# Performance work log

Hardware: AMD Instinct MI355X
Metric: run time of the kernel (lower is better)

The kernel has to match this reference:

```python
import jax, jax.numpy as jnp
import numpy as np

K = 32
BN_EPS = 1e-5


def _edgeconv(x, W, b):
    # x: [N, f] one point cloud; dynamic kNN in feature space (self included,
    # matching torch_geometric knn), edge feature [x_i, x_j - x_i], linear MLP,
    # max aggregation over the k neighbors.
    sq = jnp.sum(x * x, axis=1)                      # [N]
    dist = sq[:, None] + sq[None, :] - 2.0 * (x @ x.T)  # [N, N] squared dists
    _, idx = jax.lax.top_k(-dist, K)                 # [N, K] nearest (incl. self)
    xj = x[idx]                                      # [N, K, f]
    xi = jnp.broadcast_to(x[:, None, :], xj.shape)   # [N, K, f]
    e = jnp.concatenate([xi, xj - xi], axis=-1)      # [N, K, 2f]
    m = jnp.einsum('nkf,fo->nko', e, W) + b          # [N, K, o]
    return jnp.max(m, axis=1)                        # [N, o]


def _relu_bn(y, gamma, beta):
    # Sequential(ReLU(), BatchNorm1d(o)) in training mode over flattened nodes.
    a = jax.nn.relu(y)                               # [B, N, o]
    B, N, o = a.shape
    flat = a.reshape(B * N, o)
    mean = jnp.mean(flat, axis=0)
    var = jnp.var(flat, axis=0)
    norm = (flat - mean) * jax.lax.rsqrt(var + BN_EPS)
    return (norm * gamma + beta).reshape(B, N, o)


def setup_inputs() -> dict:
    key = jax.random.key(0)
    ks = jax.random.split(key, 4)
    B, N, fin = 8, 4096, 3
    x = jax.random.normal(ks[0], (B, N, fin), dtype=jnp.float32)
    target = jax.random.normal(ks[1], (B, N, fin), dtype=jnp.float32)
    # MLP(2*i, o) weights for layer dims (3->64), (64->64), (64->3)
    W1 = jax.random.normal(ks[2], (6, 64), dtype=jnp.float32) * (1.0 / np.sqrt(6))
    b1 = jnp.zeros((64,), jnp.float32)
    g1 = jnp.ones((64,), jnp.float32)
    be1 = jnp.zeros((64,), jnp.float32)
    W2 = jax.random.normal(ks[3], (128, 64), dtype=jnp.float32) * (1.0 / np.sqrt(128))
    b2 = jnp.zeros((64,), jnp.float32)
    g2 = jnp.ones((64,), jnp.float32)
    be2 = jnp.zeros((64,), jnp.float32)
    W3 = jax.random.normal(jax.random.fold_in(key, 7), (128, 3), dtype=jnp.float32) * (1.0 / np.sqrt(128))
    b3 = jnp.zeros((3,), jnp.float32)
    return {"x": x, "target": target, "W1": W1, "b1": b1, "g1": g1, "be1": be1,
            "W2": W2, "b2": b2, "g2": g2, "be2": be2, "W3": W3, "b3": b3}


def reference(x, target, W1, b1, g1, be1, W2, b2, g2, be2, W3, b3):
    ec = jax.vmap(_edgeconv, in_axes=(0, None, None))
    h = ec(x, W1, b1)                 # [B, N, 64]
    h = _relu_bn(h, g1, be1)
    h = ec(h, W2, b2)                 # [B, N, 64]
    h = _relu_bn(h, g2, be2)
    h = ec(h, W3, b3)                 # [B, N, 3], last activation = Identity
    loss = jnp.mean((h - target) ** 2)
    return (h, loss)
```

## Files before the change

kernel.cpp:

```cpp
#include <hip/hip_runtime.h>
#include <cstdint>
#include <cstddef>

static constexpr int NPTS  = 4096;
static constexpr int NB    = 8;
static constexpr int NROWS = NB * NPTS;
static constexpr int KNN   = 32;
static constexpr int CAP   = 256;
static constexpr int HCAP  = 128;

typedef __attribute__((ext_vector_type(8))) short  bf16x8;
typedef __attribute__((ext_vector_type(4))) float  f32x4;

__device__ __forceinline__ unsigned long long shfl_xor_u64(unsigned long long v, int m) {
  int lo = __shfl_xor((int)(unsigned)(v & 0xFFFFFFFFULL), m, 64);
  int hi = __shfl_xor((int)(unsigned)(v >> 32), m, 64);
  return ((unsigned long long)(unsigned)hi << 32) | (unsigned)lo;
}
__device__ __forceinline__ unsigned long long shfl_u64(unsigned long long v, int src) {
  int lo = __shfl((int)(unsigned)(v & 0xFFFFFFFFULL), src, 64);
  int hi = __shfl((int)(unsigned)(v >> 32), src, 64);
  return ((unsigned long long)(unsigned)hi << 32) | (unsigned)lo;
}

__device__ __forceinline__ unsigned f2o(float f) {
  unsigned u = __float_as_uint(f);
  return (u & 0x80000000u) ? ~u : (u | 0x80000000u);
}
__device__ __forceinline__ float o2f(unsigned o) {
  unsigned u = (o & 0x80000000u) ? (o ^ 0x80000000u) : ~o;
  return __uint_as_float(u);
}

__global__ __launch_bounds__(256) void sqnorm_kernel(const float* __restrict__ x,
                                                     float* __restrict__ sq, int F) {
  int t = blockIdx.x * 256 + threadIdx.x;
  if (t >= NROWS) return;
  const float* p = x + (size_t)t * F;
  float s = 0.f;
  for (int f = 0; f < F; ++f) s = fmaf(p[f], p[f], s);
  sq[t] = s;
}

__global__ __launch_bounds__(256) void split_kernel(const float* __restrict__ x,
                                                    unsigned short* __restrict__ hi,
                                                    unsigned short* __restrict__ lo,
                                                    int total) {
  int t = blockIdx.x * 256 + threadIdx.x;
  if (t >= total) return;
  float v = x[t];
  unsigned u = __float_as_uint(v);
  unsigned h = (u + 0x7FFFu + ((u >> 16) & 1u)) >> 16;
  float hf = __uint_as_float(h << 16);
  float r = v - hf;
  unsigned ur = __float_as_uint(r);
  unsigned l = (ur + 0x7FFFu + ((ur >> 16) & 1u)) >> 16;
  hi[t] = (unsigned short)h;
  lo[t] = (unsigned short)l;
}

__global__ __launch_bounds__(256) void batchmax_kernel(const float* __restrict__ sq,
                                                       float* __restrict__ sqmax) {
  int b = blockIdx.x, t = threadIdx.x;
  float m = 0.f;
  for (int i = t; i < NPTS; i += 256) m = fmaxf(m, sq[b * NPTS + i]);
  for (int off = 32; off >= 1; off >>= 1) m = fmaxf(m, __shfl_xor(m, off, 64));
  __shared__ float ls[4];
  if ((t & 63) == 0) ls[t >> 6] = m;
  __syncthreads();
  if (t == 0) sqmax[b] = fmaxf(fmaxf(ls[0], ls[1]), fmaxf(ls[2], ls[3]));
}

__global__ __launch_bounds__(256, 4)
void knn_screen(const unsigned short* __restrict__ hi,
                const unsigned short* __restrict__ lo,
                const float* __restrict__ sq,
                const float* __restrict__ sqmax,
                int* __restrict__ gcnt,
                unsigned short* __restrict__ glist) {
  constexpr int FPS = 72;
  __shared__ __attribute__((aligned(16))) unsigned short chi[128 * FPS];
  __shared__ __attribute__((aligned(16))) unsigned short clo[128 * FPS];
  __shared__ float csq[128];

  const int t = threadIdx.x, wave = t >> 6, lane = t & 63;
  const int l16 = lane & 15, quad = lane >> 4;
  const int bid = blockIdx.x;
  const int b    = bid & 7;
  const int half = (bid >> 3) & 1;
  const int i0w  = ((bid >> 4) << 6) + (wave << 4);
  const int cb   = half << 11;
  const size_t base = (size_t)b * NPTS;
  const unsigned short* hib = hi + base * 64;
  const unsigned short* lob = lo + base * 64;
  const float* sqb = sq + base;
  const float sqm = sqmax[b];

  bf16x8 ahi[2], alo[2];
#pragma unroll
  for (int kb = 0; kb < 2; ++kb) {
    ahi[kb] = *(const bf16x8*)(hib + (size_t)(i0w + l16) * 64 + kb * 32 + quad * 8);
    alo[kb] = *(const bf16x8*)(lob + (size_t)(i0w + l16) * 64 + kb * 32 + quad * 8);
  }
  float sqi4[4];
#pragma unroll
  for (int reg = 0; reg < 4; ++reg) sqi4[reg] = sqb[i0w + quad * 4 + reg];

  float t1[4], t2[4], t3[4], t4[4], tinf4[4];
  int cnt4[4] = {0, 0, 0, 0};
#pragma unroll
  for (int reg = 0; reg < 4; ++reg) {
    t1[reg] = 3.4e38f; t2[reg] = 3.4e38f; t3[reg] = 3.4e38f; t4[reg] = 3.4e38f;
    tinf4[reg] = 0.f;
  }

  for (int pass = 0; pass < 2; ++pass) {
    for (int tile = 0; tile < 16; ++tile) {
      __syncthreads();
#pragma unroll
      for (int p = 0; p < 4; ++p) {
        int id = t + p * 256;
        int r = id >> 3, c = id & 7;
        *(bf16x8*)&chi[r * FPS + c * 8] =
            *(const bf16x8*)(hib + (size_t)(cb + tile * 128 + r) * 64 + c * 8);
        *(bf16x8*)&clo[r * FPS + c * 8] =
            *(const bf16x8*)(lob + (size_t)(cb + tile * 128 + r) * 64 + c * 8);
      }
      if (t < 128) csq[t] = sqb[cb + tile * 128 + t];
      __syncthreads();

#pragma unroll 2
      for (int sub = 0; sub < 8; ++sub) {
        const int jl = sub * 16 + l16;
        bf16x8 bh0 = *(const bf16x8*)&chi[jl * FPS + quad * 8];
        bf16x8 bh1 = *(const bf16x8*)&chi[jl * FPS + 32 + quad * 8];
        bf16x8 bl0 = *(const bf16x8*)&clo[jl * FPS + quad * 8];
        bf16x8 bl1 = *(const bf16x8*)&clo[jl * FPS + 32 + quad * 8];
        f32x4 acc = {0.f, 0.f, 0.f, 0.f};
        acc = __builtin_amdgcn_mfma_f32_16x16x32_bf16(ahi[0], bh0, acc, 0, 0, 0);
        acc = __builtin_amdgcn_mfma_f32_16x16x32_bf16(ahi[1], bh1, acc, 0, 0, 0);
        acc = __builtin_amdgcn_mfma_f32_16x16x32_bf16(ahi[0], bl0, acc, 0, 0, 0);
        acc = __builtin_amdgcn_mfma_f32_16x16x32_bf16(ahi[1], bl1, acc, 0, 0, 0);
        acc = __builtin_amdgcn_mfma_f32_16x16x32_bf16(alo[0], bh0, acc, 0, 0, 0);
        acc = __builtin_amdgcn_mfma_f32_16x16x32_bf16(alo[1], bh1, acc, 0, 0, 0);
        const float cs = csq[jl];
        const int jg = cb + tile * 128 + jl;
#pragma unroll
        for (int reg = 0; reg < 4; ++reg) {
          float d = fmaf(-2.f, acc[reg], sqi4[reg] + cs);
          if (pass == 0) {
            float m1 = fminf(d,  t1[reg]); float M1 = fmaxf(d,  t1[reg]);
            float m2 = fminf(M1, t2[reg]); float M2 = fmaxf(M1, t2[reg]);
            float m3 = fminf(M2, t3[reg]); float M3 = fmaxf(M2, t3[reg]);
            t1[reg] = m1; t2[reg] = m2; t3[reg] = m3;
            t4[reg] = fminf(M3, t4[reg]);
          } else {
            bool keep = d <= tinf4[reg];
            unsigned long long mask = __ballot(keep);
            unsigned qm = (unsigned)((mask >> (quad * 16)) & 0xFFFFULL);
            int rank = __popc(qm & ((1u << l16) - 1u));
            if (keep) {
              int pos = cnt4[reg] + rank;
              if (pos < HCAP)
                glist[(size_t)(base + i0w + quad * 4 + reg) * CAP + half * HCAP + pos] =
                    (unsigned short)jg;
            }
            cnt4[reg] += __popc(qm);
          }
        }
      }
    }
    if (pass == 0) {
#pragma unroll
      for (int reg = 0; reg < 4; ++reg) {
        unsigned c0s = f2o(t1[reg]);
        unsigned c1s = f2o(t2[reg]);
        unsigned c2s = f2o(t3[reg]);
        unsigned c3s = f2o(t4[reg]);
        unsigned prefix = 0;
        int need = 32;
        for (int bit = 31; bit >= 0; --bit) {
          unsigned hm = (bit == 31) ? 0u : ~((1u << (bit + 1)) - 1u);
          bool a0 = (((c0s ^ prefix) & hm) == 0u) && (((c0s >> bit) & 1u) == 0u);
          bool a1 = (((c1s ^ prefix) & hm) == 0u) && (((c1s >> bit) & 1u) == 0u);
          bool a2 = (((c2s ^ prefix) & hm) == 0u) && (((c2s >> bit) & 1u) == 0u);
          bool a3 = (((c3s ^ prefix) & hm) == 0u) && (((c3s >> bit) & 1u) == 0u);
          unsigned long long b0 = __ballot(a0);
          unsigned long long b1 = __ballot(a1);
          unsigned long long b2 = __ballot(a2);
          unsigned long long b3 = __ballot(a3);
          int cnt0 = __popc((unsigned)((b0 >> (quad * 16)) & 0xFFFFULL))
                   + __popc((unsigned)((b1 >> (quad * 16)) & 0xFFFFULL))
                   + __popc((unsigned)((b2 >> (quad * 16)) & 0xFFFFULL))
                   + __popc((unsigned)((b3 >> (quad * 16)) & 0xFFFFULL));
          if (cnt0 < need) { need -= cnt0; prefix |= 1u << bit; }
        }
        float T = o2f(prefix);
        float eps = 6e-5f * (sqi4[reg] + sqm) + 1e-5f;
        tinf4[reg] = T + 2.f * eps;
      }
    }
  }

  if (l16 == 0) {
#pragma unroll
    for (int reg = 0; reg < 4; ++reg)
      gcnt[(base + i0w + quad * 4 + reg) * 2 + half] = cnt4[reg];
  }
}

__global__ __launch_bounds__(256, 2)
void knn_rerank(const float* __restrict__ x, const float* __restrict__ sq,
                const int* __restrict__ gcnt,
                const unsigned short* __restrict__ glist,
                unsigned short* __restrict__ idx_out) {
  const int t = threadIdx.x, wave = t >> 6, lane = t & 63;
  const int row = blockIdx.x * 4 + wave;
  const int b = row >> 12;
  const int i = row & (NPTS - 1);
  const float* xb  = x + (size_t)b * NPTS * 64;
  const float* sqb = sq + ((size_t)b << 12);

  const int n0 = gcnt[row * 2];
  const int n1 = gcnt[row * 2 + 1];
  if (n0 > HCAP || n1 > HCAP) return;

  const float sqi = sqb[i];
  float4 q[16];
#pragma unroll
  for (int c4 = 0; c4 < 16; ++c4)
    q[c4] = *(const float4*)(xb + (size_t)i * 64 + c4 * 4);

  const int n = n0 + n1;
  unsigned long long vk[4];
#pragma unroll
  for (int s = 0; s < 4; ++s) {
    int li = s * 64 + lane;
    unsigned long long v = 0xFFFFFFFFFFFULL;
    if (li < n) {
      int sl = (li < n0) ? li : (HCAP + (li - n0));
      int j = glist[(size_t)row * CAP + sl];
      const float4* xj = (const float4*)(xb + (size_t)j * 64);
      float dot = 0.f;
#pragma unroll
      for (int c4 = 0; c4 < 16; ++c4) {
        float4 c = xj[c4];
        dot = fmaf(q[c4].x, c.x, dot);
        dot = fmaf(q[c4].y, c.y, dot);
        dot = fmaf(q[c4].z, c.z, dot);
        dot = fmaf(q[c4].w, c.w, dot);
      }
      float d = fmaf(-2.f, dot, sqi + sqb[j]);
      unsigned u  = __float_as_uint(d);
      unsigned ck = (u & 0x80000000u) ? ~u : (u | 0x80000000u);
      v = ((unsigned long long)ck << 12) | (unsigned)j;
    }
    vk[s] = v;
  }
  unsigned long long prefix = 0;
  int need = 32;
  for (int bit = 43; bit >= 0; --bit) {
    unsigned long long hm = (bit == 43) ? 0ULL
        : (~((1ULL << (bit + 1)) - 1ULL) & 0xFFFFFFFFFFFULL);
    int cnt0 = 0;
#pragma unroll
    for (int s = 0; s < 4; ++s) {
      bool a = ((vk[s] ^ prefix) & hm) == 0ULL;
      bool z = ((vk[s] >> bit) & 1ULL) == 0ULL;
      cnt0 += (int)__popcll(__ballot(a && z));
    }
    if (cnt0 < need) { need -= cnt0; prefix |= 1ULL << bit; }
  }
  int prev = 0;
#pragma unroll
  for (int s = 0; s < 4; ++s) {
    bool sel = vk[s] <= prefix;
    unsigned long long m = __ballot(sel);
    int rank = (int)__popcll(m & ((1ULL << lane) - 1ULL));
    if (sel)
      idx_out[(size_t)row * KNN + prev + rank] =
          (unsigned short)(vk[s] & 0xFFFULL);
    prev += (int)__popcll(m);
  }
}

__global__ __launch_bounds__(256)
void knn_rerank_fb(const float* __restrict__ x, const float* __restrict__ sq,
                   const int* __restrict__ gcnt,
                   unsigned short* __restrict__ idx_out) {
  __shared__ unsigned long long fsurv[4][128];
  const int t = threadIdx.x, wave = t >> 6, lane = t & 63;
  const int row = blockIdx.x * 4 + wave;
  const int b = row >> 12;
  const int i = row & (NPTS - 1);

  const int n0 = gcnt[row * 2];
  const int n1 = gcnt[row * 2 + 1];
  if (n0 <= HCAP && n1 <= HCAP) return;

  const float* xb  = x + (size_t)b * NPTS * 64;
  const float* sqb = sq + ((size_t)b << 12);
  const float sqi = sqb[i];

  float4 q[16];
#pragma unroll
  for (int c4 = 0; c4 < 16; ++c4)
    q[c4] = *(const float4*)(xb + (size_t)i * 64 + c4 * 4);

  unsigned mnf = 0xFFFFFFFFu;
  for (int c0 = 0; c0 < NPTS; c0 += 64) {
    const int j = c0 + lane;
    const float4* xj = (const float4*)(xb + (size_t)j * 64);
    float dot = 0.f;
#pragma unroll
    for (int c4 = 0; c4 < 16; ++c4) {
      float4 c = xj[c4];
      dot = fmaf(q[c4].x, c.x, dot);
      dot = fmaf(q[c4].y, c.y, dot);
      dot = fmaf(q[c4].z, c.z, dot);
      dot = fmaf(q[c4].w, c.w, dot);
    }
    float d = fmaf(-2.f, dot, sqi + sqb[j]);
    unsigned u  = __float_as_uint(d);
    unsigned ck = (u & 0x80000000u) ? ~u : (u | 0x80000000u);
    mnf = ck < mnf ? ck : mnf;
  }
  unsigned tau32;
  {
    const unsigned v = mnf;
    unsigned prefix32 = 0;
    int need = 32;
    int act = 1;
    for (int bit = 31; bit >= 0; --bit) {
      const unsigned bv = (v >> bit) & 1u;
      unsigned long long m0 = __ballot(act && (bv == 0u));
      int c0n = (int)__popcll(m0);
      if (c0n >= need) {
        act = act && (bv == 0u);
      } else {
        need -= c0n;
        act = act && (bv == 1u);
        prefix32 |= (1u << bit);
      }
    }
    tau32 = prefix32;
  }
  int cnt = 0;
  for (int c0 = 0; c0 < NPTS; c0 += 64) {
    const int j = c0 + lane;
    const float4* xj = (const float4*)(xb + (size_t)j * 64);
    float dot = 0.f;
#pragma unroll
    for (int c4 = 0; c4 < 16; ++c4) {
      float4 c = xj[c4];
      dot = fmaf(q[c4].x, c.x, dot);
      dot = fmaf(q[c4].y, c.y, dot);
      dot = fmaf(q[c4].z, c.z, dot);
      dot = fmaf(q[c4].w, c.w, dot);
    }
    float d = fmaf(-2.f, dot, sqi + sqb[j]);
    unsigned u  = __float_as_uint(d);
    unsigned ck = (u & 0x80000000u) ? ~u : (u | 0x80000000u);
    bool keep = ck <= tau32;
    unsigned long long mask = __ballot(keep);
    if (mask != 0ULL) {
      int rank = (int)__popcll(mask & ((1ULL << lane) - 1ULL));
      if (keep) {
        int pos = cnt + rank;
        if (pos < 128)
          fsurv[wave][pos] = ((unsigned long long)ck << 12) | (unsigned)j;
      }
      cnt += (int)__popcll(mask);
    }
  }
  if (cnt <= 128) {
    unsigned long long vk0 = (lane      < cnt) ? fsurv[wave][lane]      : 0xFFFFFFFFFFFULL;
    unsigned long long vk1 = (lane + 64 < cnt) ? fsurv[wave][lane + 64] : 0xFFFFFFFFFFFULL;
    unsigned long long prefix = 0;
    int need = 32;
    for (int bit = 43; bit >= 0; --bit) {
      unsigned long long hm = (bit == 43) ? 0ULL
          : (~((1ULL << (bit + 1)) - 1ULL) & 0xFFFFFFFFFFFULL);
      bool a0 = (((vk0 ^ prefix) & hm) == 0ULL) && (((vk0 >> bit) & 1ULL) == 0ULL);
      bool a1 = (((vk1 ^ prefix) & hm) == 0ULL) && (((vk1 >> bit) & 1ULL) == 0ULL);
      int cnt0 = (int)__popcll(__ballot(a0)) + (int)__popcll(__ballot(a1));
      if (cnt0 < need) { need -= cnt0; prefix |= 1ULL << bit; }
    }
    bool sel0 = vk0 <= prefix;
    unsigned long long m0 = __ballot(sel0);
    int rank0 = (int)__popcll(m0 & ((1ULL << lane) - 1ULL));
    if (sel0)
      idx_out[(size_t)row * KNN + rank0] = (unsigned short)(vk0 & 0xFFFULL);
    int prev = (int)__popcll(m0);
    bool sel1 = vk1 <= prefix;
    unsigned long long m1 = __ballot(sel1);
    int rank1 = (int)__popcll(m1 & ((1ULL << lane) - 1ULL));
    if (sel1)
      idx_out[(size_t)row * KNN + prev + rank1] = (unsigned short)(vk1 & 0xFFFULL);
  } else {
    unsigned long long ent = (0xFFFFFFFFFFFULL << 5) | (unsigned long long)(lane & 31);
    unsigned long long M   = (0xFFFFFFFFFFFULL << 5) | 31ULL;
    for (int c0 = 0; c0 < NPTS; c0 += 64) {
      const int j = c0 + lane;
      const float4* xj = (const float4*)(xb + (size_t)j * 64);
      float dot = 0.f;
#pragma unroll
      for (int c4 = 0; c4 < 16; ++c4) {
        float4 c = xj[c4];
        dot = fmaf(q[c4].x, c.x, dot);
        dot = fmaf(q[c4].y, c.y, dot);
        dot = fmaf(q[c4].z, c.z, dot);
        dot = fmaf(q[c4].w, c.w, dot);
      }
      float d = fmaf(-2.f, dot, sqi + sqb[j]);
      unsigned u  = __float_as_uint(d);
      unsigned ck = (u & 0x80000000u) ? ~u : (u | 0x80000000u);
      unsigned long long cq = ((unsigned long long)ck << 12) | (unsigned)j;
      unsigned long long mask = __ballot(cq < (M >> 5));
      while (mask) {
        const int src = __builtin_ctzll(mask);
        mask &= mask - 1;
        const unsigned long long bq = shfl_u64(cq, src);
        if (bq < (M >> 5)) {
          const unsigned slot = (unsigned)(M & 31ULL);
          if ((unsigned)(lane & 31) == slot) ent = (bq << 5) | slot;
          unsigned long long v = ent;
#pragma unroll
          for (int off = 16; off >= 1; off >>= 1) {
            unsigned long long w2 = shfl_xor_u64(v, off);
            v = (v > w2) ? v : w2;
          }
          M = v;
        }
      }
    }
    if (lane < 32)
      idx_out[(size_t)row * KNN + lane] =
          (unsigned short)((ent >> 5) & 0xFFFULL);
  }
}

template <int F>
__global__ __launch_bounds__(256, 4) void knn_tiled(const float* __restrict__ x,
                                                    const float* __restrict__ sq,
                                                    unsigned short* __restrict__ idx_out) {
  constexpr int FP = 4;
  constexpr int TC = 256;
  constexpr int RPB = 32;
  constexpr int RPW = 8;
  constexpr int SCAP = 128;

  __shared__ __attribute__((aligned(16))) float qv[RPB][FP];
  __shared__ float qsq[RPB];
  __shared__ __attribute__((aligned(16))) float ct[TC][FP];
  __shared__ float csq[TC];
  __shared__ unsigned long long surv[RPB][SCAP];

  const int t    = threadIdx.x;
  const int wave = t >> 6;
  const int lane = t & 63;
  const int rowbase = blockIdx.x << 5;
  const int b     = rowbase >> 12;
  const int ibase = rowbase & (NPTS - 1);
  const float* xb  = x + (size_t)b * NPTS * F;
  const float* sqb = sq + (b << 12);

  if (t < RPB) {
    qv[t][0] = xb[(size_t)(ibase + t) * 3 + 0];
    qv[t][1] = xb[(size_t)(ibase + t) * 3 + 1];
    qv[t][2] = xb[(size_t)(ibase + t) * 3 + 2];
    qv[t][3] = 0.f;
    qsq[t] = sqb[ibase + t];
  }
  __syncthreads();

  const int r0 = wave << 3;
  float4 q[RPW];
  float sqi[RPW];
#pragma unroll
  for (int rr = 0; rr < RPW; ++rr) {
    q[rr] = *reinterpret_cast<const float4*>(&qv[r0 + rr][0]);
    sqi[rr] = qsq[r0 + rr];
  }

  unsigned mn[RPW];
#pragma unroll
  for (int rr = 0; rr < RPW; ++rr) mn[rr] = 0xFFFFFFFFu;

  for (int tile = 0; tile < NPTS / TC; ++tile) {
    __syncthreads();
    {
      int jg = tile * TC + t;
      ct[t][0] = xb[(size_t)jg * 3 + 0];
      ct[t][1] = xb[(size_t)jg * 3 + 1];
      ct[t][2] = xb[(size_t)jg * 3 + 2];
      ct[t][3] = 0.f;
      csq[t] = sqb[jg];
    }
    __syncthreads();

    float4 c0 = *reinterpret_cast<const float4*>(&ct[lane][0]);
    float4 c1 = *reinterpret_cast<const float4*>(&ct[lane + 64][0]);
    float4 c2 = *reinterpret_cast<const float4*>(&ct[lane + 128][0]);
    float4 c3 = *reinterpret_cast<const float4*>(&ct[lane + 192][0]);
    float cs[4];
#pragma unroll
    for (int s = 0; s < 4; ++s) cs[s] = csq[lane + 64 * s];

#pragma unroll
    for (int rr = 0; rr < RPW; ++rr) {
      float4 qq = q[rr];
      float dd[4];
      dd[0] = fmaf(qq.z, c0.z, fmaf(qq.y, c0.y, qq.x * c0.x));
      dd[1] = fmaf(qq.z, c1.z, fmaf(qq.y, c1.y, qq.x * c1.x));
      dd[2] = fmaf(qq.z, c2.z, fmaf(qq.y, c2.y, qq.x * c2.x));
      dd[3] = fmaf(qq.z, c3.z, fmaf(qq.y, c3.y, qq.x * c3.x));
#pragma unroll
      for (int s = 0; s < 4; ++s) {
        float d = fmaf(-2.f, dd[s], sqi[rr] + cs[s]);
        unsigned u  = __float_as_uint(d);
        unsigned ck = (u & 0x80000000u) ? ~u : (u | 0x80000000u);
        mn[rr] = ck < mn[rr] ? ck : mn[rr];
      }
    }
  }

  unsigned tau[RPW];
#pragma unroll
  for (int rr = 0; rr < RPW; ++rr) {
    const unsigned v = mn[rr];
    unsigned prefix = 0;
    int need = 32;
    int act = 1;
    for (int bit = 31; bit >= 0; --bit) {
      const unsigned bv = (v >> bit) & 1u;
      unsigned long long m0 = __ballot(act && (bv == 0u));
      int c0n = (int)__popcll(m0);
      if (c0n >= need) {
        act = act && (bv == 0u);
      } else {
        need -= c0n;
        act = act && (bv == 1u);
        prefix |= (1u << bit);
      }
    }
    tau[rr] = prefix;
  }

  int cnt[RPW];
#pragma unroll
  for (int rr = 0; rr < RPW; ++rr) cnt[rr] = 0;

  for (int tile = 0; tile < NPTS / TC; ++tile) {
    __syncthreads();
    {
      int jg = tile * TC + t;
      ct[t][0] = xb[(size_t)jg * 3 + 0];
      ct[t][1] = xb[(size_t)jg * 3 + 1];
      ct[t][2] = xb[(size_t)jg * 3 + 2];
      ct[t][3] = 0.f;
      csq[t] = sqb[jg];
    }
    __syncthreads();

    float4 c0 = *reinterpret_cast<const float4*>(&ct[lane][0]);
    float4 c1 = *reinterpret_cast<const float4*>(&ct[lane + 64][0]);
    float4 c2 = *reinterpret_cast<const float4*>(&ct[lane + 128][0]);
    float4 c3 = *reinterpret_cast<const float4*>(&ct[lane + 192][0]);
    float cs[4];
#pragma unroll
    for (int s = 0; s < 4; ++s) cs[s] = csq[lane + 64 * s];

#pragma unroll
    for (int rr = 0; rr < RPW; ++rr) {
      float4 qq = q[rr];
      float dd[4];
      dd[0] = fmaf(qq.z, c0.z, fmaf(qq.y, c0.y, qq.x * c0.x));
      dd[1] = fmaf(qq.z, c1.z, fmaf(qq.y, c1.y, qq.x * c1.x));
      dd[2] = fmaf(qq.z, c2.z, fmaf(qq.y, c2.y, qq.x * c2.x));
      dd[3] = fmaf(qq.z, c3.z, fmaf(qq.y, c3.y, qq.x * c3.x));
#pragma unroll
      for (int s = 0; s < 4; ++s) {
        float d = fmaf(-2.f, dd[s], sqi[rr] + cs[s]);
        unsigned u  = __float_as_uint(d);
        unsigned ck = (u & 0x80000000u) ? ~u : (u | 0x80000000u);
        bool keep = ck <= tau[rr];
        unsigned long long mask = __ballot(keep);
        if (mask != 0ULL) {
          int rank = (int)__popcll(mask & ((1ULL << lane) - 1ULL));
          if (keep) {
            int pos = cnt[rr] + rank;
            if (pos < SCAP)
              surv[r0 + rr][pos] =
                  ((unsigned long long)ck << 12) |
                  (unsigned)(tile * TC + s * 64 + lane);
          }
          cnt[rr] += (int)__popcll(mask);
        }
      }
    }
  }

#pragma unroll
  for (int rr = 0; rr < RPW; ++rr) {
    const int row = rowbase + r0 + rr;
    const int n = cnt[rr];
    if (n <= SCAP) {
      unsigned long long vk0 = (lane      < n) ? surv[r0 + rr][lane]      : 0xFFFFFFFFFFFULL;
      unsigned long long vk1 = (lane + 64 < n) ? surv[r0 + rr][lane + 64] : 0xFFFFFFFFFFFULL;
      unsigned long long prefix = 0;
      int need = 32;
      for (int bit = 43; bit >= 0; --bit) {
        unsigned long long hm = (bit == 43) ? 0ULL
            : (~((1ULL << (bit + 1)) - 1ULL) & 0xFFFFFFFFFFFULL);
        bool a0 = (((vk0 ^ prefix) & hm) == 0ULL) && (((vk0 >> bit) & 1ULL) == 0ULL);
        bool a1 = (((vk1 ^ prefix) & hm) == 0ULL) && (((vk1 >> bit) & 1ULL) == 0ULL);
        int cnt0 = (int)__popcll(__ballot(a0)) + (int)__popcll(__ballot(a1));
        if (cnt0 < need) { need -= cnt0; prefix |= 1ULL << bit; }
      }
      bool sel0 = vk0 <= prefix;
      unsigned long long m0 = __ballot(sel0);
      int rank0 = (int)__popcll(m0 & ((1ULL << lane) - 1ULL));
      if (sel0)
        idx_out[(row << 5) + rank0] = (unsigned short)(vk0 & 0xFFFULL);
      int prev = (int)__popcll(m0);
      bool sel1 = vk1 <= prefix;
      unsigned long long m1 = __ballot(sel1);
      int rank1 = (int)__popcll(m1 & ((1ULL << lane) - 1ULL));
      if (sel1)
        idx_out[(row << 5) + prev + rank1] = (unsigned short)(vk1 & 0xFFFULL);
    } else {
      unsigned long long ent = (0xFFFFFFFFFFFULL << 5) | (unsigned long long)(lane & 31);
      unsigned long long M   = (0xFFFFFFFFFFFULL << 5) | 31ULL;
      const float4 qq = q[rr];
      const float si = sqi[rr];
      for (int c0i = 0; c0i < NPTS; c0i += 64) {
        const int j = c0i + lane;
        const float dd_ = fmaf(qq.z, xb[(size_t)j * 3 + 2],
                           fmaf(qq.y, xb[(size_t)j * 3 + 1],
                                qq.x * xb[(size_t)j * 3 + 0]));
        float d = fmaf(-2.f, dd_, si + sqb[j]);
        unsigned u  = __float_as_uint(d);
        unsigned ck = (u & 0x80000000u) ? ~u : (u | 0x80000000u);
        unsigned long long cq = ((unsigned long long)ck << 12) | (unsigned)j;
        unsigned long long mask = __ballot(cq < (M >> 5));
        while (mask) {
          const int src = __builtin_ctzll(mask);
          mask &= mask - 1;
          const unsigned long long bq = shfl_u64(cq, src);
          if (bq < (M >> 5)) {
            const unsigned slot = (unsigned)(M & 31ULL);
            if ((unsigned)(lane & 31) == slot) ent = (bq << 5) | slot;
            unsigned long long v = ent;
#pragma unroll
            for (int off = 16; off >= 1; off >>= 1) {
              unsigned long long w2 = shfl_xor_u64(v, off);
              v = (v > w2) ? v : w2;
            }
            M = v;
          }
        }
      }
      if (lane < 32)
        idx_out[(row << 5) + lane] = (unsigned short)((ent >> 5) & 0xFFFULL);
    }
  }
}

__global__ __launch_bounds__(256) void mlp_pc_kernel(const float* __restrict__ xin,
                                                     const float* __restrict__ W,
                                                     const float* __restrict__ bias,
                                                     float* __restrict__ P,
                                                     float* C,
                                                     int F, int O, int total) {
  int t = blockIdx.x * 256 + threadIdx.x;
  if (t >= total) return;
  int n = t / O, o = t % O;
  const float* xr = xin + (size_t)n * F;
  const float* Wt = W + o;
  const float* Wb = W + (size_t)F * O + o;
  float p = 0.f, c = 0.f;
  for (int f = 0; f < F; ++f) {
    float a  = xr[f];
    float wt = Wt[(size_t)f * O];
    float wb = Wb[(size_t)f * O];
    p = fmaf(a, wb, p);
    c = fmaf(a, wt - wb, c);
  }
  P[t] = p;
  C[t] = c + bias[o];
}

__global__ __launch_bounds__(256) void aggregate_kernel(const unsigned short* __restrict__ idx,
                                                        const float* __restrict__ P,
                                                        float* h, int O, int total) {
  int t = blockIdx.x * 256 + threadIdx.x;
  if (t >= total) return;
  int n = t / O, o = t % O;
  const unsigned short* ix = idx + (size_t)n * KNN;
  const int rowbase = (n >> 12) << 12;
  float m = -3.402823466e+38f;
  for (int k = 0; k < KNN; ++k) {
    int jg = rowbase + ix[k];
    float v = P[(size_t)jg * O + o];
    m = fmaxf(m, v);
  }
  h[t] = h[t] + m;
}

__global__ __launch_bounds__(256) void bn_stats_kernel(const float* __restrict__ h,
                                                       float* __restrict__ stats) {
  const int c = blockIdx.x;
  const int t = threadIdx.x;
  double s = 0.0, s2 = 0.0;
  for (int n = t; n < NROWS; n += 256) {
    float v = h[(size_t)n * 64 + c];
    v = v > 0.f ? v : 0.f;
    s += v;
    s2 += (double)v * v;
  }
  __shared__ double ls[256], ls2[256];
  ls[t] = s; ls2[t] = s2;
  __syncthreads();
  for (int st = 128; st; st >>= 1) {
    if (t < st) { ls[t] += ls[t + st]; ls2[t] += ls2[t + st]; }
    __syncthreads();
  }
  if (t == 0) {
    double mean = ls[0] / (double)NROWS;
    double var  = ls2[0] / (double)NROWS - mean * mean;
    stats[c]      = (float)mean;
    stats[64 + c] = (float)(1.0 / sqrt(var + 1e-5));
  }
}

__global__ __launch_bounds__(256) void bn_apply_kernel(const float* h,
                                                       const float* __restrict__ stats,
                                                       const float* __restrict__ g,
                                                       const float* __restrict__ be,
                                                       float* out, int total) {
  int t = blockIdx.x * 256 + threadIdx.x;
  if (t >= total) return;
  int ch = t & 63;
  float v = fmaxf(h[t], 0.f);
  out[t] = (v - stats[ch]) * stats[64 + ch] * g[ch] + be[ch];
}

__global__ __launch_bounds__(256) void final_kernel(const float* __restrict__ h3,
                                                    const float* __restrict__ target,
                                                    float* __restrict__ out,
                                                    double* __restrict__ partial) {
  double s = 0.0;
  for (int t = blockIdx.x * 256 + threadIdx.x; t < NROWS * 3; t += 256 * 256) {
    float v = h3[t];
    out[t] = v;
    float d = v - target[t];
    s += (double)d * d;
  }
  __shared__ double ls[256];
  int t = threadIdx.x;
  ls[t] = s;
  __syncthreads();
  for (int st = 128; st; st >>= 1) {
    if (t < st) ls[t] += ls[t + st];
    __syncthreads();
  }
  if (t == 0) partial[blockIdx.x] = ls[0];
}

__global__ __launch_bounds__(256) void loss_kernel(const double* __restrict__ partial,
                                                   float* __restrict__ out) {
  int t = threadIdx.x;
  __shared__ double ls[256];
  ls[t] = partial[t];
  __syncthreads();
  for (int st = 128; st; st >>= 1) {
    if (t < st) ls[t] += ls[t + st];
    __syncthreads();
  }
  if (t == 0) out[NROWS * 3] = (float)(ls[0] / (double)(NROWS * 3));
}

extern "C" void kernel_launch(void* const* d_in, const int* in_sizes, int n_in,
                              void* d_out, int out_size, void* d_ws, size_t ws_size,
                              hipStream_t stream) {
  const float* x   = (const float*)d_in[0];
  const float* tgt = (const float*)d_in[1];
  const float* W1  = (const float*)d_in[2];
  const float* b1  = (const float*)d_in[3];
  const float* g1  = (const float*)d_in[4];
  const float* be1 = (const float*)d_in[5];
  const float* W2  = (const float*)d_in[6];
  const float* b2  = (const float*)d_in[7];
  const float* g2  = (const float*)d_in[8];
  const float* be2 = (const float*)d_in[9];
  const float* W3  = (const float*)d_in[10];
  const float* b3  = (const float*)d_in[11];
  float* out = (float*)d_out;

  char* ws = (char*)d_ws;
  size_t off = 0;
  float* sq    = (float*)(ws + off); off += (size_t)NROWS * 4;
  unsigned short* idxb = (unsigned short*)(ws + off); off += (size_t)NROWS * KNN * 2;
  float* P     = (float*)(ws + off); off += (size_t)NROWS * 64 * 4;
  float* CA    = (float*)(ws + off); off += (size_t)NROWS * 64 * 4;
  float* CB    = (float*)(ws + off); off += (size_t)NROWS * 64 * 4;
  int*   gcnt  = (int*)(ws + off);   off += (size_t)NROWS * 8;
  unsigned short* glist = (unsigned short*)(ws + off); off += (size_t)NROWS * CAP * 2;
  float* stats = (float*)(ws + off); off += 256 * 4;
  float* sqmax = (float*)(ws + off); off += 64;
  double* part = (double*)(ws + off); off += 256 * 8;

  unsigned short* hib = (unsigned short*)P;
  unsigned short* lob = hib + (size_t)NROWS * 64;

  const int T64 = NROWS * 64;
  const int T3  = NROWS * 3;

  sqnorm_kernel<<<NROWS / 256, 256, 0, stream>>>(x, sq, 3);
  knn_tiled<3><<<NROWS / 32, 256, 0, stream>>>(x, sq, idxb);
  mlp_pc_kernel<<<T64 / 256, 256, 0, stream>>>(x, W1, b1, P, CA, 3, 64, T64);
  aggregate_kernel<<<T64 / 256, 256, 0, stream>>>(idxb, P, CA, 64, T64);
  bn_stats_kernel<<<64, 256, 0, stream>>>(CA, stats);
  bn_apply_kernel<<<T64 / 256, 256, 0, stream>>>(CA, stats, g1, be1, CA, T64);

  sqnorm_kernel<<<NROWS / 256, 256, 0, stream>>>(CA, sq, 64);
  split_kernel<<<T64 / 256, 256, 0, stream>>>(CA, hib, lob, T64);
  batchmax_kernel<<<NB, 256, 0, stream>>>(sq, sqmax);
  knn_screen<<<1024, 256, 0, stream>>>(hib, lob, sq, sqmax, gcnt, glist);
  knn_rerank<<<NROWS / 4, 256, 0, stream>>>(CA, sq, gcnt, glist, idxb);
  knn_rerank_fb<<<NROWS / 4, 256, 0, stream>>>(CA, sq, gcnt, idxb);
  mlp_pc_kernel<<<T64 / 256, 256, 0, stream>>>(CA, W2, b2, P, CB, 64, 64, T64);
  aggregate_kernel<<<T64 / 256, 256, 0, stream>>>(idxb, P, CB, 64, T64);
  bn_stats_kernel<<<64, 256, 0, stream>>>(CB, stats);
  bn_apply_kernel<<<T64 / 256, 256, 0, stream>>>(CB, stats, g2, be2, CB, T64);

  sqnorm_kernel<<<NROWS / 256, 256, 0, stream>>>(CB, sq, 64);
  split_kernel<<<T64 / 256, 256, 0, stream>>>(CB, hib, lob, T64);
  batchmax_kernel<<<NB, 256, 0, stream>>>(sq, sqmax);
  knn_screen<<<1024, 256, 0, stream>>>(hib, lob, sq, sqmax, gcnt, glist);
  knn_rerank<<<NROWS / 4, 256, 0, stream>>>(CB, sq, gcnt, glist, idxb);
  knn_rerank_fb<<<NROWS / 4, 256, 0, stream>>>(CB, sq, gcnt, idxb);
  mlp_pc_kernel<<<T3 / 256, 256, 0, stream>>>(CB, W3, b3, P, CA, 64, 3, T3);
  aggregate_kernel<<<T3 / 256, 256, 0, stream>>>(idxb, P, CA, 3, T3);

  final_kernel<<<256, 256, 0, stream>>>(CA, tgt, out, part);
  loss_kernel<<<1, 256, 0, stream>>>(part, out);
}
```

Baseline: 1.312 ms.

## Split kNN screen into quarter candidate ranges and drop LDS tiling

```diff
diff --git a/kernel.cpp b/kernel.cpp
--- a/kernel.cpp
+++ b/kernel.cpp
@@ -6,8 +6,8 @@
 static constexpr int NB    = 8;
 static constexpr int NROWS = NB * NPTS;
 static constexpr int KNN   = 32;
-static constexpr int CAP   = 256;
-static constexpr int HCAP  = 128;
+static constexpr int CAP   = 384;
+static constexpr int QCAP  = 96;
 
 typedef __attribute__((ext_vector_type(8))) short  bf16x8;
 typedef __attribute__((ext_vector_type(4))) float  f32x4;
@@ -71,25 +71,20 @@
   if (t == 0) sqmax[b] = fmaxf(fmaxf(ls[0], ls[1]), fmaxf(ls[2], ls[3]));
 }
 
-__global__ __launch_bounds__(256, 4)
+__global__ __launch_bounds__(256, 6)
 void knn_screen(const unsigned short* __restrict__ hi,
                 const unsigned short* __restrict__ lo,
                 const float* __restrict__ sq,
                 const float* __restrict__ sqmax,
                 int* __restrict__ gcnt,
                 unsigned short* __restrict__ glist) {
-  constexpr int FPS = 72;
-  __shared__ __attribute__((aligned(16))) unsigned short chi[128 * FPS];
-  __shared__ __attribute__((aligned(16))) unsigned short clo[128 * FPS];
-  __shared__ float csq[128];
-
   const int t = threadIdx.x, wave = t >> 6, lane = t & 63;
   const int l16 = lane & 15, quad = lane >> 4;
   const int bid = blockIdx.x;
   const int b    = bid & 7;
-  const int half = (bid >> 3) & 1;
-  const int i0w  = ((bid >> 4) << 6) + (wave << 4);
-  const int cb   = half << 11;
+  const int qtr  = (bid >> 3) & 3;
+  const int i0w  = ((bid >> 5) << 6) + (wave << 4);
+  const int cbq  = qtr << 10;
   const size_t base = (size_t)b * NPTS;
   const unsigned short* hib = hi + base * 64;
   const unsigned short* lob = lo + base * 64;
@@ -114,90 +109,93 @@
     tinf4[reg] = 0.f;
   }
 
-  for (int pass = 0; pass < 2; ++pass) {
-    for (int tile = 0; tile < 16; ++tile) {
-      __syncthreads();
-#pragma unroll
-      for (int p = 0; p < 4; ++p) {
-        int id = t + p * 256;
-        int r = id >> 3, c = id & 7;
-        *(bf16x8*)&chi[r * FPS + c * 8] =
-            *(const bf16x8*)(hib + (size_t)(cb + tile * 128 + r) * 64 + c * 8);
-        *(bf16x8*)&clo[r * FPS + c * 8] =
-            *(const bf16x8*)(lob + (size_t)(cb + tile * 128 + r) * 64 + c * 8);
-      }
-      if (t < 128) csq[t] = sqb[cb + tile * 128 + t];
-      __syncthreads();
-
-#pragma unroll 2
-      for (int sub = 0; sub < 8; ++sub) {
-        const int jl = sub * 16 + l16;
-        bf16x8 bh0 = *(const bf16x8*)&chi[jl * FPS + quad * 8];
-        bf16x8 bh1 = *(const bf16x8*)&chi[jl * FPS + 32 + quad * 8];
-        bf16x8 bl0 = *(const bf16x8*)&clo[jl * FPS + quad * 8];
-        bf16x8 bl1 = *(const bf16x8*)&clo[jl * FPS + 32 + quad * 8];
-        f32x4 acc = {0.f, 0.f, 0.f, 0.f};
-        acc = __builtin_amdgcn_mfma_f32_16x16x32_bf16(ahi[0], bh0, acc, 0, 0, 0);
-        acc = __builtin_amdgcn_mfma_f32_16x16x32_bf16(ahi[1], bh1, acc, 0, 0, 0);
-        acc = __builtin_amdgcn_mfma_f32_16x16x32_bf16(ahi[0], bl0, acc, 0, 0, 0);
-        acc = __builtin_amdgcn_mfma_f32_16x16x32_bf16(ahi[1], bl1, acc, 0, 0, 0);
-        acc = __builtin_amdgcn_mfma_f32_16x16x32_bf16(alo[0], bh0, acc, 0, 0, 0);
-        acc = __builtin_amdgcn_mfma_f32_16x16x32_bf16(alo[1], bh1, acc, 0, 0, 0);
-        const float cs = csq[jl];
-        const int jg = cb + tile * 128 + jl;
-#pragma unroll
-        for (int reg = 0; reg < 4; ++reg) {
-          float d = fmaf(-2.f, acc[reg], sqi4[reg] + cs);
-          if (pass == 0) {
-            float m1 = fminf(d,  t1[reg]); float M1 = fmaxf(d,  t1[reg]);
-            float m2 = fminf(M1, t2[reg]); float M2 = fmaxf(M1, t2[reg]);
-            float m3 = fminf(M2, t3[reg]); float M3 = fmaxf(M2, t3[reg]);
-            t1[reg] = m1; t2[reg] = m2; t3[reg] = m3;
-            t4[reg] = fminf(M3, t4[reg]);
-          } else {
-            bool keep = d <= tinf4[reg];
-            unsigned long long mask = __ballot(keep);
-            unsigned qm = (unsigned)((mask >> (quad * 16)) & 0xFFFFULL);
-            int rank = __popc(qm & ((1u << l16) - 1u));
-            if (keep) {
-              int pos = cnt4[reg] + rank;
-              if (pos < HCAP)
-                glist[(size_t)(base + i0w + quad * 4 + reg) * CAP + half * HCAP + pos] =
-                    (unsigned short)jg;
-            }
-            cnt4[reg] += __popc(qm);
-          }
+  for (int sub = 0; sub < 64; ++sub) {
+    const int jg = cbq + sub * 16 + l16;
+    const unsigned short* hj = hib + (size_t)jg * 64 + quad * 8;
+    const unsigned short* lj = lob + (size_t)jg * 64 + quad * 8;
+    bf16x8 bh0 = *(const bf16x8*)(hj);
+    bf16x8 bh1 = *(const bf16x8*)(hj + 32);
+    bf16x8 bl0 = *(const bf16x8*)(lj);
+    bf16x8 bl1 = *(const bf16x8*)(lj + 32);
+    f32x4 acc = {0.f, 0.f, 0.f, 0.f};
+    acc = __builtin_amdgcn_mfma_f32_16x16x32_bf16(ahi[0], bh0, acc, 0, 0, 0);
+    acc = __builtin_amdgcn_mfma_f32_16x16x32_bf16(ahi[1], bh1, acc, 0, 0, 0);
+    acc = __builtin_amdgcn_mfma_f32_16x16x32_bf16(ahi[0], bl0, acc, 0, 0, 0);
+    acc = __builtin_amdgcn_mfma_f32_16x16x32_bf16(ahi[1], bl1, acc, 0, 0, 0);
+    acc = __builtin_amdgcn_mfma_f32_16x16x32_bf16(alo[0], bh0, acc, 0, 0, 0);
+    acc = __builtin_amdgcn_mfma_f32_16x16x32_bf16(alo[1], bh1, acc, 0, 0, 0);
+    const float cs = sqb[jg];
+#pragma unroll
+    for (int reg = 0; reg < 4; ++reg) {
+      float d = fmaf(-2.f, acc[reg], sqi4[reg] + cs);
+      float m1 = fminf(d,  t1[reg]); float M1 = fmaxf(d,  t1[reg]);
+      float m2 = fminf(M1, t2[reg]); float M2 = fmaxf(M1, t2[reg]);
+      float m3 = fminf(M2, t3[reg]); float M3 = fmaxf(M2, t3[reg]);
+      t1[reg] = m1; t2[reg] = m2; t3[reg] = m3;
+      t4[reg] = fminf(M3, t4[reg]);
+    }
+  }
+
+#pragma unroll
+  for (int reg = 0; reg < 4; ++reg) {
+    unsigned c0s = f2o(t1[reg]);
+    unsigned c1s = f2o(t2[reg]);
+    unsigned c2s = f2o(t3[reg]);
+    unsigned c3s = f2o(t4[reg]);
+    unsigned prefix = 0;
+    int need = 32;
+    for (int bit = 31; bit >= 0; --bit) {
+      unsigned hm = (bit == 31) ? 0u : ~((1u << (bit + 1)) - 1u);
+      bool a0 = (((c0s ^ prefix) & hm) == 0u) && (((c0s >> bit) & 1u) == 0u);
+      bool a1 = (((c1s ^ prefix) & hm) == 0u) && (((c1s >> bit) & 1u) == 0u);
+      bool a2 = (((c2s ^ prefix) & hm) == 0u) && (((c2s >> bit) & 1u) == 0u);
+      bool a3 = (((c3s ^ prefix) & hm) == 0u) && (((c3s >> bit) & 1u) == 0u);
+      unsigned long long b0 = __ballot(a0);
+      unsigned long long b1 = __ballot(a1);
+      unsigned long long b2 = __ballot(a2);
+      unsigned long long b3 = __ballot(a3);
+      int cnt0 = __popc((unsigned)((b0 >> (quad * 16)) & 0xFFFFULL))
+               + __popc((unsigned)((b1 >> (quad * 16)) & 0xFFFFULL))
+               + __popc((unsigned)((b2 >> (quad * 16)) & 0xFFFFULL))
+               + __popc((unsigned)((b3 >> (quad * 16)) & 0xFFFFULL));
+      if (cnt0 < need) { need -= cnt0; prefix |= 1u << bit; }
+    }
+    float T = o2f(prefix);
+    float eps = 6e-5f * (sqi4[reg] + sqm) + 1e-5f;
+    tinf4[reg] = T + 2.f * eps;
+  }
+
+  for (int sub = 0; sub < 64; ++sub) {
+    const int jg = cbq + sub * 16 + l16;
+    const unsigned short* hj = hib + (size_t)jg * 64 + quad * 8;
+    const unsigned short* lj = lob + (size_t)jg * 64 + quad * 8;
+    bf16x8 bh0 = *(const bf16x8*)(hj);
+    bf16x8 bh1 = *(const bf16x8*)(hj + 32);
+    bf16x8 bl0 = *(const bf16x8*)(lj);
+    bf16x8 bl1 = *(const bf16x8*)(lj + 32);
+    f32x4 acc = {0.f, 0.f, 0.f, 0.f};
+    acc = __builtin_amdgcn_mfma_f32_16x16x32_bf16(ahi[0], bh0, acc, 0, 0, 0);
+    acc = __builtin_amdgcn_mfma_f32_16x16x32_bf16(ahi[1], bh1, acc, 0, 0, 0);
+    acc = __builtin_amdgcn_mfma_f32_16x16x32_bf16(ahi[0], bl0, acc, 0, 0, 0);
+    acc = __builtin_amdgcn_mfma_f32_16x16x32_bf16(ahi[1], bl1, acc, 0, 0, 0);
+    acc = __builtin_amdgcn_mfma_f32_16x16x32_bf16(alo[0], bh0, acc, 0, 0, 0);
+    acc = __builtin_amdgcn_mfma_f32_16x16x32_bf16(alo[1], bh1, acc, 0, 0, 0);
+    const float cs = sqb[jg];
+#pragma unroll
+    for (int reg = 0; reg < 4; ++reg) {
+      float d = fmaf(-2.f, acc[reg], sqi4[reg] + cs);
+      bool keep = d <= tinf4[reg];
+      unsigned long long mask = __ballot(keep);
+      unsigned qm = (unsigned)((mask >> (quad * 16)) & 0xFFFFULL);
+      if (qm) {
+        int rank = __popc(qm & ((1u << l16) - 1u));
+        if (keep) {
+          int pos = cnt4[reg] + rank;
+          if (pos < QCAP)
+            glist[(size_t)(base + i0w + quad * 4 + reg) * CAP + qtr * QCAP + pos] =
+                (unsigned short)jg;
         }
-      }
-    }
-    if (pass == 0) {
-#pragma unroll
-      for (int reg = 0; reg < 4; ++reg) {
-        unsigned c0s = f2o(t1[reg]);
-        unsigned c1s = f2o(t2[reg]);
-        unsigned c2s = f2o(t3[reg]);
-        unsigned c3s = f2o(t4[reg]);
-        unsigned prefix = 0;
-        int need = 32;
-        for (int bit = 31; bit >= 0; --bit) {
-          unsigned hm = (bit == 31) ? 0u : ~((1u << (bit + 1)) - 1u);
-          bool a0 = (((c0s ^ prefix) & hm) == 0u) && (((c0s >> bit) & 1u) == 0u);
-          bool a1 = (((c1s ^ prefix) & hm) == 0u) && (((c1s >> bit) & 1u) == 0u);
-          bool a2 = (((c2s ^ prefix) & hm) == 0u) && (((c2s >> bit) & 1u) == 0u);
-          bool a3 = (((c3s ^ prefix) & hm) == 0u) && (((c3s >> bit) & 1u) == 0u);
-          unsigned long long b0 = __ballot(a0);
-          unsigned long long b1 = __ballot(a1);
-          unsigned long long b2 = __ballot(a2);
-          unsigned long long b3 = __ballot(a3);
-          int cnt0 = __popc((unsigned)((b0 >> (quad * 16)) & 0xFFFFULL))
-                   + __popc((unsigned)((b1 >> (quad * 16)) & 0xFFFFULL))
-                   + __popc((unsigned)((b2 >> (quad * 16)) & 0xFFFFULL))
-                   + __popc((unsigned)((b3 >> (quad * 16)) & 0xFFFFULL));
-          if (cnt0 < need) { need -= cnt0; prefix |= 1u << bit; }
-        }
-        float T = o2f(prefix);
-        float eps = 6e-5f * (sqi4[reg] + sqm) + 1e-5f;
-        tinf4[reg] = T + 2.f * eps;
+        cnt4[reg] += __popc(qm);
       }
     }
   }
@@ -205,7 +203,7 @@
   if (l16 == 0) {
 #pragma unroll
     for (int reg = 0; reg < 4; ++reg)
-      gcnt[(base + i0w + quad * 4 + reg) * 2 + half] = cnt4[reg];
+      gcnt[(base + i0w + quad * 4 + reg) * 4 + qtr] = cnt4[reg];
   }
 }
 
@@ -221,9 +219,11 @@
   const float* xb  = x + (size_t)b * NPTS * 64;
   const float* sqb = sq + ((size_t)b << 12);
 
-  const int n0 = gcnt[row * 2];
-  const int n1 = gcnt[row * 2 + 1];
-  if (n0 > HCAP || n1 > HCAP) return;
+  const int n0 = gcnt[row * 4 + 0];
+  const int n1 = gcnt[row * 4 + 1];
+  const int n2 = gcnt[row * 4 + 2];
+  const int n3 = gcnt[row * 4 + 3];
+  if (n0 > QCAP || n1 > QCAP || n2 > QCAP || n3 > QCAP) return;
 
   const float sqi = sqb[i];
   float4 q[16];
@@ -231,14 +231,19 @@
   for (int c4 = 0; c4 < 16; ++c4)
     q[c4] = *(const float4*)(xb + (size_t)i * 64 + c4 * 4);
 
-  const int n = n0 + n1;
-  unsigned long long vk[4];
-#pragma unroll
-  for (int s = 0; s < 4; ++s) {
+  const int n01  = n0 + n1;
+  const int n012 = n01 + n2;
+  const int n    = n012 + n3;
+  unsigned long long vk[6];
+#pragma unroll
+  for (int s = 0; s < 6; ++s) {
     int li = s * 64 + lane;
     unsigned long long v = 0xFFFFFFFFFFFULL;
     if (li < n) {
-      int sl = (li < n0) ? li : (HCAP + (li - n0));
+      int sl = (li < n0)   ? li
+             : (li < n01)  ? QCAP     + (li - n0)
+             : (li < n012) ? 2 * QCAP + (li - n01)
+                           : 3 * QCAP + (li - n012);
       int j = glist[(size_t)row * CAP + sl];
       const float4* xj = (const float4*)(xb + (size_t)j * 64);
       float dot = 0.f;
@@ -264,7 +269,7 @@
         : (~((1ULL << (bit + 1)) - 1ULL) & 0xFFFFFFFFFFFULL);
     int cnt0 = 0;
 #pragma unroll
-    for (int s = 0; s < 4; ++s) {
+    for (int s = 0; s < 6; ++s) {
       bool a = ((vk[s] ^ prefix) & hm) == 0ULL;
       bool z = ((vk[s] >> bit) & 1ULL) == 0ULL;
       cnt0 += (int)__popcll(__ballot(a && z));
@@ -273,7 +278,7 @@
   }
   int prev = 0;
 #pragma unroll
-  for (int s = 0; s < 4; ++s) {
+  for (int s = 0; s < 6; ++s) {
     bool sel = vk[s] <= prefix;
     unsigned long long m = __ballot(sel);
     int rank = (int)__popcll(m & ((1ULL << lane) - 1ULL));
@@ -294,9 +299,11 @@
   const int b = row >> 12;
   const int i = row & (NPTS - 1);
 
-  const int n0 = gcnt[row * 2];
-  const int n1 = gcnt[row * 2 + 1];
-  if (n0 <= HCAP && n1 <= HCAP) return;
+  const int n0 = gcnt[row * 4 + 0];
+  const int n1 = gcnt[row * 4 + 1];
+  const int n2 = gcnt[row * 4 + 2];
+  const int n3 = gcnt[row * 4 + 3];
+  if (n0 <= QCAP && n1 <= QCAP && n2 <= QCAP && n3 <= QCAP) return;
 
   const float* xb  = x + (size_t)b * NPTS * 64;
   const float* sqb = sq + ((size_t)b << 12);
@@ -805,7 +812,7 @@
   float* P     = (float*)(ws + off); off += (size_t)NROWS * 64 * 4;
   float* CA    = (float*)(ws + off); off += (size_t)NROWS * 64 * 4;
   float* CB    = (float*)(ws + off); off += (size_t)NROWS * 64 * 4;
-  int*   gcnt  = (int*)(ws + off);   off += (size_t)NROWS * 8;
+  int*   gcnt  = (int*)(ws + off);   off += (size_t)NROWS * 16;
   unsigned short* glist = (unsigned short*)(ws + off); off += (size_t)NROWS * CAP * 2;
   float* stats = (float*)(ws + off); off += 256 * 4;
   float* sqmax = (float*)(ws + off); off += 64;
@@ -827,7 +834,7 @@
   sqnorm_kernel<<<NROWS / 256, 256, 0, stream>>>(CA, sq, 64);
   split_kernel<<<T64 / 256, 256, 0, stream>>>(CA, hib, lob, T64);
   batchmax_kernel<<<NB, 256, 0, stream>>>(sq, sqmax);
-  knn_screen<<<1024, 256, 0, stream>>>(hib, lob, sq, sqmax, gcnt, glist);
+  knn_screen<<<2048, 256, 0, stream>>>(hib, lob, sq, sqmax, gcnt, glist);
   knn_rerank<<<NROWS / 4, 256, 0, stream>>>(CA, sq, gcnt, glist, idxb);
   knn_rerank_fb<<<NROWS / 4, 256, 0, stream>>>(CA, sq, gcnt, idxb);
   mlp_pc_kernel<<<T64 / 256, 256, 0, stream>>>(CA, W2, b2, P, CB, 64, 64, T64);
@@ -838,7 +845,7 @@
   sqnorm_kernel<<<NROWS / 256, 256, 0, stream>>>(CB, sq, 64);
   split_kernel<<<T64 / 256, 256, 0, stream>>>(CB, hib, lob, T64);
   batchmax_kernel<<<NB, 256, 0, stream>>>(sq, sqmax);
-  knn_screen<<<1024, 256, 0, stream>>>(hib, lob, sq, sqmax, gcnt, glist);
+  knn_screen<<<2048, 256, 0, stream>>>(hib, lob, sq, sqmax, gcnt, glist);
   knn_rerank<<<NROWS / 4, 256, 0, stream>>>(CB, sq, gcnt, glist, idxb);
   knn_rerank_fb<<<NROWS / 4, 256, 0, stream>>>(CB, sq, gcnt, idxb);
   mlp_pc_kernel<<<T3 / 256, 256, 0, stream>>>(CB, W3, b3, P, CA, 64, 3, T3);
```

New measurement: 2.024 ms. 1.54x slower.
